# Kernel optimization log

Measured on AMD Instinct MI355X. Metric: run time of the kernel, lower is better.

Reference implementation:

```python
import jax, jax.numpy as jnp
import numpy as np

SIZE = 32
NUM_CLASSES = 10
B = 16384
RTOL = 0.01
ATOL = 0.01
MAX_STEPS = 96
H0 = 0.05


def setup_inputs() -> dict:
    key = jax.random.key(0)
    ks = jax.random.split(key, 9)
    p = lambda k, s: 0.1 * jax.random.normal(k, s, dtype=jnp.float32)
    z = lambda n: jnp.zeros((n,), dtype=jnp.float32)
    x = jax.random.normal(ks[0], (B, 2), dtype=jnp.float32)
    # per-sample ODE end times T_i in (0, 3]
    samples = 3.0 * jax.random.uniform(ks[1], (B, 1), dtype=jnp.float32) + 1e-3
    return dict(
        x=x, samples=samples,
        node_w1=p(ks[2], (3, SIZE)), node_b1=z(SIZE),
        node_w2=p(ks[3], (SIZE, SIZE)), node_b2=z(SIZE),
        node_w3=p(ks[4], (SIZE, 2)), node_b3=z(2),
        fc_w=p(ks[5], (2, NUM_CLASSES)), fc_b=z(NUM_CLASSES),
        enc_w1=p(ks[6], (2, SIZE)), enc_b1=z(SIZE),
        enc_w2=p(ks[7], (SIZE, SIZE)), enc_b2=z(SIZE),
        enc_w3=p(ks[8], (SIZE, 2)), enc_b3=z(2),
    )


def _net_forward(x, samples, node_w1, node_b1, node_w2, node_b2, node_w3, node_b3,
                 fc_w, fc_b, enc_w1, enc_b1, enc_w2, enc_b2, enc_w3, enc_b3):
    # Encoder -> (alpha, beta) feed only the external prob_model (no effect on act_vec)
    h = jax.nn.relu(x @ enc_w1 + enc_b1)
    h = jax.nn.relu(h @ enc_w2 + enc_b2)
    ab = h @ enc_w3 + enc_b3
    alpha, beta = jnp.exp(ab[:, 0]), jnp.exp(ab[:, 1])  # unused downstream (side effects only)

    # samples[samples >= 50] = 50
    T = jnp.minimum(samples[:, 0], 50.0)  # [B] per-sample end times

    def f(t, y):  # NODE dynamics; t: [B], y: [B,2]
        zin = jnp.concatenate([t[:, None], y], axis=1)  # [B,3]
        h1 = jax.nn.relu(zin @ node_w1 + node_b1)
        h2 = jax.nn.relu(h1 @ node_w2 + node_b2)
        return h2 @ node_w3 + node_b3  # [B,2]

    def step(carry, _):
        t, y, hstep = carry
        rem = T - t
        active = rem > 1e-8
        hs = jnp.where(active, jnp.minimum(hstep, rem), 0.0)  # never overshoot T
        hb = hs[:, None]
        # Dopri5 (RK45) stages
        k1 = f(t, y)
        k2 = f(t + hs * 0.2, y + hb * (0.2 * k1))
        k3 = f(t + hs * 0.3, y + hb * (3.0 / 40.0 * k1 + 9.0 / 40.0 * k2))
        k4 = f(t + hs * 0.8, y + hb * (44.0 / 45.0 * k1 - 56.0 / 15.0 * k2 + 32.0 / 9.0 * k3))
        k5 = f(t + hs * (8.0 / 9.0), y + hb * (19372.0 / 6561.0 * k1 - 25360.0 / 2187.0 * k2 + 64448.0 / 6561.0 * k3 - 212.0 / 729.0 * k4))
        k6 = f(t + hs, y + hb * (9017.0 / 3168.0 * k1 - 355.0 / 33.0 * k2 + 46732.0 / 5247.0 * k3 + 49.0 / 176.0 * k4 - 5103.0 / 18656.0 * k5))
        y5 = y + hb * (35.0 / 384.0 * k1 + 500.0 / 1113.0 * k3 + 125.0 / 192.0 * k4 - 2187.0 / 6784.0 * k5 + 11.0 / 84.0 * k6)
        k7 = f(t + hs, y5)
        err = hb * (71.0 / 57600.0 * k1 - 71.0 / 16695.0 * k3 + 71.0 / 1920.0 * k4 - 17253.0 / 339200.0 * k5 + 22.0 / 525.0 * k6 - 1.0 / 40.0 * k7)
        scale = ATOL + RTOL * jnp.maximum(jnp.abs(y), jnp.abs(y5))
        en = jnp.sqrt(jnp.mean((err / scale) ** 2, axis=1))  # [B]
        accept = active & (en <= 1.0)
        fac = jnp.clip(0.9 * jnp.maximum(en, 1e-10) ** (-0.2), 0.2, 10.0)
        t_n = jnp.where(accept, t + hs, t)
        y_n = jnp.where(accept[:, None], y5, y)
        h_n = jnp.where(active, hs * fac, hstep)
        return (t_n, y_n, h_n), None

    t0 = jnp.zeros((x.shape[0],), dtype=x.dtype)
    h0 = jnp.full((x.shape[0],), H0, dtype=x.dtype)
    (tF, yF, hF), _ = jax.lax.scan(step, (t0, x, h0), None, length=MAX_STEPS)

    # temp[idx] = flow of x[idx] from t=0 to its own T[idx] (sort/scatter in the
    # original only routes each sample's own interpolated state back to its row)
    act = yF @ fc_w + fc_b  # [B, num_classes]
    return act[None, :, :]  # act_vec: [1, B, num_classes]


def reference(x, samples, node_w1, node_b1, node_w2, node_b2, node_w3, node_b3,
              fc_w, fc_b, enc_w1, enc_b1, enc_w2, enc_b2, enc_w3, enc_b3):
    return _net_forward(x, samples, node_w1, node_b1, node_w2, node_b2, node_w3, node_b3,
                        fc_w, fc_b, enc_w1, enc_b1, enc_w2, enc_b2, enc_w3, enc_b3)
```

## Files before the change

kernel.cpp:

```cpp
#include <hip/hip_runtime.h>
#include <math.h>


#define MAXS 96

typedef float v2f __attribute__((ext_vector_type(2)));

static __device__ __forceinline__ v2f splat(float s) { v2f v; v.x = s; v.y = s; return v; }
static __device__ __forceinline__ v2f vfma(v2f a, v2f b, v2f c) { return __builtin_elementwise_fma(a, b, c); }
static __device__ __forceinline__ v2f vrelu(v2f a) { return __builtin_elementwise_max(a, splat(0.0f)); }

template<int CTRL>
static __device__ __forceinline__ float dppf(float x) {
    return __int_as_float(__builtin_amdgcn_update_dpp(
        0, __float_as_int(x), CTRL, 0xF, 0xF, false));
}

static __device__ __forceinline__ v2f dpp_allreduce16(v2f p) {
    p.x += dppf<0xB1>(p.x);  p.y += dppf<0xB1>(p.y);
    p.x += dppf<0x4E>(p.x);  p.y += dppf<0x4E>(p.y);
    p.x += dppf<0x141>(p.x); p.y += dppf<0x141>(p.y);
    p.x += dppf<0x140>(p.x); p.y += dppf<0x140>(p.y);
    return p;
}

__global__ __launch_bounds__(256, 3) void node_kernel(
    const float* __restrict__ x, const float* __restrict__ samples,
    const float* __restrict__ w1, const float* __restrict__ b1,
    const float* __restrict__ w2, const float* __restrict__ b2,
    const float* __restrict__ w3, const float* __restrict__ b3,
    const float* __restrict__ fcw, const float* __restrict__ fcb,
    float* __restrict__ out, int n)
{
    const int tid  = blockIdx.x * blockDim.x + threadIdx.x;
    const int elem = tid >> 4;
    const int m    = tid & 15;
    if (elem >= n) return;

    __shared__ float lds[16 * 36];
    float* slot = &lds[(threadIdx.x >> 4) * 36];

    const v2f* w1v = (const v2f*)w1;
    const v2f* b1v = (const v2f*)b1;
    const v2f* w2v = (const v2f*)w2;
    const v2f* b2v = (const v2f*)b2;
    const v2f* w3v = (const v2f*)w3;

    v2f w1r0 = w1v[0 * 16 + m];
    v2f w1r1 = w1v[1 * 16 + m];
    v2f w1r2 = w1v[2 * 16 + m];
    v2f b1c  = b1v[m];
    v2f b2c  = b2v[m];
    v2f w3r0 = w3v[2 * m + 0];
    v2f w3r1 = w3v[2 * m + 1];
    v2f b3c  = { b3[0], b3[1] };

    v2f w2c[32];
#pragma unroll
    for (int i = 0; i < 32; ++i) w2c[i] = w2v[i * 16 + m];

#pragma unroll
    for (int i = 0; i < 32; ++i) { asm volatile("" : "+v"(w2c[i])); }
    asm volatile("" : "+v"(w1r0), "+v"(w1r1), "+v"(w1r2), "+v"(b1c), "+v"(b2c));
    asm volatile("" : "+v"(w3r0), "+v"(w3r1));

    v2f y = ((const v2f*)x)[elem];
    float T = fminf(samples[elem], 50.0f);
    float t = 0.0f;
    float h = 0.05f;

    auto f_eval = [&](float tt, v2f z) -> v2f {
        v2f hv = vfma(splat(tt), w1r0, vfma(splat(z.x), w1r1,
                 vfma(splat(z.y), w1r2, b1c)));
        hv = vrelu(hv);

        ((v2f*)slot)[m] = hv;

        const float4* gp = (const float4*)slot;
        float4 r0 = gp[0], r1 = gp[1], r2 = gp[2], r3 = gp[3];
        float4 r4 = gp[4], r5 = gp[5], r6 = gp[6], r7 = gp[7];

        v2f a0 = b2c, a1 = splat(0.0f), a2 = splat(0.0f), a3 = splat(0.0f);
        a0 = vfma(splat(r0.x), w2c[ 0], a0); a1 = vfma(splat(r0.y), w2c[ 1], a1);
        a2 = vfma(splat(r0.z), w2c[ 2], a2); a3 = vfma(splat(r0.w), w2c[ 3], a3);
        a0 = vfma(splat(r1.x), w2c[ 4], a0); a1 = vfma(splat(r1.y), w2c[ 5], a1);
        a2 = vfma(splat(r1.z), w2c[ 6], a2); a3 = vfma(splat(r1.w), w2c[ 7], a3);
        a0 = vfma(splat(r2.x), w2c[ 8], a0); a1 = vfma(splat(r2.y), w2c[ 9], a1);
        a2 = vfma(splat(r2.z), w2c[10], a2); a3 = vfma(splat(r2.w), w2c[11], a3);
        a0 = vfma(splat(r3.x), w2c[12], a0); a1 = vfma(splat(r3.y), w2c[13], a1);
        a2 = vfma(splat(r3.z), w2c[14], a2); a3 = vfma(splat(r3.w), w2c[15], a3);
        a0 = vfma(splat(r4.x), w2c[16], a0); a1 = vfma(splat(r4.y), w2c[17], a1);
        a2 = vfma(splat(r4.z), w2c[18], a2); a3 = vfma(splat(r4.w), w2c[19], a3);
        a0 = vfma(splat(r5.x), w2c[20], a0); a1 = vfma(splat(r5.y), w2c[21], a1);
        a2 = vfma(splat(r5.z), w2c[22], a2); a3 = vfma(splat(r5.w), w2c[23], a3);
        a0 = vfma(splat(r6.x), w2c[24], a0); a1 = vfma(splat(r6.y), w2c[25], a1);
        a2 = vfma(splat(r6.z), w2c[26], a2); a3 = vfma(splat(r6.w), w2c[27], a3);
        a0 = vfma(splat(r7.x), w2c[28], a0); a1 = vfma(splat(r7.y), w2c[29], a1);
        a2 = vfma(splat(r7.z), w2c[30], a2); a3 = vfma(splat(r7.w), w2c[31], a3);

        v2f acc = vrelu((a0 + a1) + (a2 + a3));

        v2f p = vfma(splat(acc.x), w3r0, splat(acc.y) * w3r1);
        p = dpp_allreduce16(p);
        return p + b3c;
    };

    v2f k1 = f_eval(0.0f, y);

    for (int s = 0; s < MAXS; ++s) {
        float rem = T - t;
        if (!(rem > 1e-8f)) break;
        float hs = fminf(h, rem);
        v2f hb = splat(hs);

        v2f k2 = f_eval(t + hs * 0.2f, vfma(hb, splat(0.2f) * k1, y));
        v2f k3 = f_eval(t + hs * 0.3f,
                 vfma(hb, vfma(splat((float)(3.0/40.0)), k1, splat((float)(9.0/40.0)) * k2), y));
        v2f k4 = f_eval(t + hs * 0.8f,
                 vfma(hb, vfma(splat((float)(44.0/45.0)), k1,
                          vfma(splat((float)(-56.0/15.0)), k2, splat((float)(32.0/9.0)) * k3)), y));
        v2f k5 = f_eval(t + hs * (float)(8.0/9.0),
                 vfma(hb, vfma(splat((float)(19372.0/6561.0)), k1,
                          vfma(splat((float)(-25360.0/2187.0)), k2,
                          vfma(splat((float)(64448.0/6561.0)), k3,
                               splat((float)(-212.0/729.0)) * k4))), y));
        v2f k6 = f_eval(t + hs,
                 vfma(hb, vfma(splat((float)(9017.0/3168.0)), k1,
                          vfma(splat((float)(-355.0/33.0)), k2,
                          vfma(splat((float)(46732.0/5247.0)), k3,
                          vfma(splat((float)(49.0/176.0)), k4,
                               splat((float)(-5103.0/18656.0)) * k5)))), y));
        v2f y5 = vfma(hb, vfma(splat((float)(35.0/384.0)), k1,
                          vfma(splat((float)(500.0/1113.0)), k3,
                          vfma(splat((float)(125.0/192.0)), k4,
                          vfma(splat((float)(-2187.0/6784.0)), k5,
                               splat((float)(11.0/84.0)) * k6)))), y);
        v2f k7 = f_eval(t + hs, y5);

        v2f err = hb * vfma(splat((float)(71.0/57600.0)), k1,
                       vfma(splat((float)(-71.0/16695.0)), k3,
                       vfma(splat((float)(71.0/1920.0)), k4,
                       vfma(splat((float)(-17253.0/339200.0)), k5,
                       vfma(splat((float)(22.0/525.0)), k6,
                            splat((float)(-1.0/40.0)) * k7)))));

        v2f ay  = __builtin_elementwise_abs(y);
        v2f ay5 = __builtin_elementwise_abs(y5);
        v2f sc  = vfma(splat(0.01f), __builtin_elementwise_max(ay, ay5), splat(0.01f));
        v2f r   = err / sc;
        float en = sqrtf(0.5f * (r.x * r.x + r.y * r.y));

        float fac = 0.9f * powf(fmaxf(en, 1e-10f), -0.2f);
        fac = fminf(fmaxf(fac, 0.2f), 10.0f);

        bool accept = (en <= 1.0f);
        if (accept) { t += hs; y = y5; }
        k1 = accept ? k7 : k1;
        h = hs * fac;
    }

    if (m < 10) {
        out[10 * elem + m] = fmaf(y.x, fcw[m], fmaf(y.y, fcw[10 + m], fcb[m]));
    }
}

extern "C" void kernel_launch(void* const* d_in, const int* in_sizes, int n_in,
                              void* d_out, int out_size, void* d_ws, size_t ws_size,
                              hipStream_t stream) {
    const float* x   = (const float*)d_in[0];
    const float* sm  = (const float*)d_in[1];
    const float* w1  = (const float*)d_in[2];
    const float* b1  = (const float*)d_in[3];
    const float* w2  = (const float*)d_in[4];
    const float* b2  = (const float*)d_in[5];
    const float* w3  = (const float*)d_in[6];
    const float* b3  = (const float*)d_in[7];
    const float* fcw = (const float*)d_in[8];
    const float* fcb = (const float*)d_in[9];
    float* out = (float*)d_out;

    int n = in_sizes[1];
    const int block = 256;
    long long threads = (long long)n * 16;
    int grid = (int)((threads + block - 1) / block);
    node_kernel<<<grid, block, 0, stream>>>(x, sm, w1, b1, w2, b2, w3, b3,
                                            fcw, fcb, out, n);
}
```

Before: 105.6 us.

## Map each sample to 8 lanes with DPP quad broadcast plus LDS half-exchange

Each ODE sample is now handled by 8 lanes instead of 16, with each lane computing 4 hidden units and holding twice as many w2 weights in registers. Half of the hidden vector is gathered with DPP quad broadcasts and the other half is read from LDS, and the final reduction drops one DPP stage. This halves the total thread count and the per-sample duplicated step-control arithmetic, at the cost of much higher register use (occupancy hint lowered to 2) and a longer serial FMA chain per lane. The step-factor powf is replaced by exp2f/log2f.

Result: faster. 101.0 us, median of 2 (-4.4%).

```diff
diff --git a/kernel.cpp b/kernel.cpp
--- a/kernel.cpp
+++ b/kernel.cpp
@@ -6,25 +6,22 @@
 
 typedef float v2f __attribute__((ext_vector_type(2)));
 
-static __device__ __forceinline__ v2f splat(float s) { v2f v; v.x = s; v.y = s; return v; }
-static __device__ __forceinline__ v2f vfma(v2f a, v2f b, v2f c) { return __builtin_elementwise_fma(a, b, c); }
-static __device__ __forceinline__ v2f vrelu(v2f a) { return __builtin_elementwise_max(a, splat(0.0f)); }
+static __device__ __forceinline__ v2f splat(float s){ v2f v; v.x=s; v.y=s; return v; }
+static __device__ __forceinline__ v2f vfma(v2f a, v2f b, v2f c){ return __builtin_elementwise_fma(a,b,c); }
+static __device__ __forceinline__ v2f vrelu(v2f a){ return __builtin_elementwise_max(a, splat(0.0f)); }
 
 template<int CTRL>
-static __device__ __forceinline__ float dppf(float x) {
-    return __int_as_float(__builtin_amdgcn_update_dpp(
-        0, __float_as_int(x), CTRL, 0xF, 0xF, false));
-}
-
-static __device__ __forceinline__ v2f dpp_allreduce16(v2f p) {
+static __device__ __forceinline__ float dppf(float x){
+    return __int_as_float(__builtin_amdgcn_update_dpp(0, __float_as_int(x), CTRL, 0xF, 0xF, false));
+}
+static __device__ __forceinline__ v2f dpp_allreduce8(v2f p){
     p.x += dppf<0xB1>(p.x);  p.y += dppf<0xB1>(p.y);
     p.x += dppf<0x4E>(p.x);  p.y += dppf<0x4E>(p.y);
     p.x += dppf<0x141>(p.x); p.y += dppf<0x141>(p.y);
-    p.x += dppf<0x140>(p.x); p.y += dppf<0x140>(p.y);
     return p;
 }
 
-__global__ __launch_bounds__(256, 3) void node_kernel(
+__global__ __launch_bounds__(256, 2) void node_kernel(
     const float* __restrict__ x, const float* __restrict__ samples,
     const float* __restrict__ w1, const float* __restrict__ b1,
     const float* __restrict__ w2, const float* __restrict__ b2,
@@ -33,36 +30,48 @@
     float* __restrict__ out, int n)
 {
     const int tid  = blockIdx.x * blockDim.x + threadIdx.x;
-    const int elem = tid >> 4;
-    const int m    = tid & 15;
+    const int elem = tid >> 3;
+    const int m    = tid & 7;
     if (elem >= n) return;
-
-    __shared__ float lds[16 * 36];
-    float* slot = &lds[(threadIdx.x >> 4) * 36];
-
-    const v2f* w1v = (const v2f*)w1;
-    const v2f* b1v = (const v2f*)b1;
-    const v2f* w2v = (const v2f*)w2;
-    const v2f* b2v = (const v2f*)b2;
+    const int q = m >> 2;
+
+    __shared__ float lds[32 * 36];
+    float* slot = &lds[(threadIdx.x >> 3) * 36];
+    const int mineBase  = 16 * q;
+    const int otherBase = 16 - mineBase;
+
+    const float4* w2v4 = (const float4*)w2;
+    v2f w2mA[16], w2mB[16];
+    v2f w2oA[16], w2oB[16];
+#pragma unroll
+    for (int k = 0; k < 16; ++k) {
+        float4 rm = w2v4[(mineBase  + k) * 8 + m];
+        float4 ro = w2v4[(otherBase + k) * 8 + m];
+        w2mA[k].x = rm.x; w2mA[k].y = rm.y; w2mB[k].x = rm.z; w2mB[k].y = rm.w;
+        w2oA[k].x = ro.x; w2oA[k].y = ro.y; w2oB[k].x = ro.z; w2oB[k].y = ro.w;
+    }
+    float4 w1f0 = ((const float4*)w1)[0 * 8 + m];
+    float4 w1f1 = ((const float4*)w1)[1 * 8 + m];
+    float4 w1f2 = ((const float4*)w1)[2 * 8 + m];
+    float4 b1f  = ((const float4*)b1)[m];
+    float4 b2f  = ((const float4*)b2)[m];
+    v2f w1_0A = {w1f0.x, w1f0.y}, w1_0B = {w1f0.z, w1f0.w};
+    v2f w1_1A = {w1f1.x, w1f1.y}, w1_1B = {w1f1.z, w1f1.w};
+    v2f w1_2A = {w1f2.x, w1f2.y}, w1_2B = {w1f2.z, w1f2.w};
+    v2f b1A   = {b1f.x,  b1f.y }, b1B   = {b1f.z,  b1f.w };
+    v2f b2A   = {b2f.x,  b2f.y }, b2B   = {b2f.z,  b2f.w };
     const v2f* w3v = (const v2f*)w3;
-
-    v2f w1r0 = w1v[0 * 16 + m];
-    v2f w1r1 = w1v[1 * 16 + m];
-    v2f w1r2 = w1v[2 * 16 + m];
-    v2f b1c  = b1v[m];
-    v2f b2c  = b2v[m];
-    v2f w3r0 = w3v[2 * m + 0];
-    v2f w3r1 = w3v[2 * m + 1];
+    v2f w3r0 = w3v[4*m+0], w3r1 = w3v[4*m+1], w3r2 = w3v[4*m+2], w3r3 = w3v[4*m+3];
     v2f b3c  = { b3[0], b3[1] };
 
-    v2f w2c[32];
 #pragma unroll
-    for (int i = 0; i < 32; ++i) w2c[i] = w2v[i * 16 + m];
-
-#pragma unroll
-    for (int i = 0; i < 32; ++i) { asm volatile("" : "+v"(w2c[i])); }
-    asm volatile("" : "+v"(w1r0), "+v"(w1r1), "+v"(w1r2), "+v"(b1c), "+v"(b2c));
-    asm volatile("" : "+v"(w3r0), "+v"(w3r1));
+    for (int k = 0; k < 16; ++k) {
+        asm volatile("" : "+v"(w2mA[k]), "+v"(w2mB[k]), "+v"(w2oA[k]), "+v"(w2oB[k]));
+    }
+    asm volatile("" : "+v"(w1_0A), "+v"(w1_0B), "+v"(w1_1A), "+v"(w1_1B));
+    asm volatile("" : "+v"(w1_2A), "+v"(w1_2B), "+v"(b1A), "+v"(b1B));
+    asm volatile("" : "+v"(b2A), "+v"(b2B));
+    asm volatile("" : "+v"(w3r0), "+v"(w3r1), "+v"(w3r2), "+v"(w3r3));
 
     v2f y = ((const v2f*)x)[elem];
     float T = fminf(samples[elem], 50.0f);
@@ -70,38 +79,65 @@
     float h = 0.05f;
 
     auto f_eval = [&](float tt, v2f z) -> v2f {
-        v2f hv = vfma(splat(tt), w1r0, vfma(splat(z.x), w1r1,
-                 vfma(splat(z.y), w1r2, b1c)));
-        hv = vrelu(hv);
-
-        ((v2f*)slot)[m] = hv;
-
-        const float4* gp = (const float4*)slot;
-        float4 r0 = gp[0], r1 = gp[1], r2 = gp[2], r3 = gp[3];
-        float4 r4 = gp[4], r5 = gp[5], r6 = gp[6], r7 = gp[7];
-
-        v2f a0 = b2c, a1 = splat(0.0f), a2 = splat(0.0f), a3 = splat(0.0f);
-        a0 = vfma(splat(r0.x), w2c[ 0], a0); a1 = vfma(splat(r0.y), w2c[ 1], a1);
-        a2 = vfma(splat(r0.z), w2c[ 2], a2); a3 = vfma(splat(r0.w), w2c[ 3], a3);
-        a0 = vfma(splat(r1.x), w2c[ 4], a0); a1 = vfma(splat(r1.y), w2c[ 5], a1);
-        a2 = vfma(splat(r1.z), w2c[ 6], a2); a3 = vfma(splat(r1.w), w2c[ 7], a3);
-        a0 = vfma(splat(r2.x), w2c[ 8], a0); a1 = vfma(splat(r2.y), w2c[ 9], a1);
-        a2 = vfma(splat(r2.z), w2c[10], a2); a3 = vfma(splat(r2.w), w2c[11], a3);
-        a0 = vfma(splat(r3.x), w2c[12], a0); a1 = vfma(splat(r3.y), w2c[13], a1);
-        a2 = vfma(splat(r3.z), w2c[14], a2); a3 = vfma(splat(r3.w), w2c[15], a3);
-        a0 = vfma(splat(r4.x), w2c[16], a0); a1 = vfma(splat(r4.y), w2c[17], a1);
-        a2 = vfma(splat(r4.z), w2c[18], a2); a3 = vfma(splat(r4.w), w2c[19], a3);
-        a0 = vfma(splat(r5.x), w2c[20], a0); a1 = vfma(splat(r5.y), w2c[21], a1);
-        a2 = vfma(splat(r5.z), w2c[22], a2); a3 = vfma(splat(r5.w), w2c[23], a3);
-        a0 = vfma(splat(r6.x), w2c[24], a0); a1 = vfma(splat(r6.y), w2c[25], a1);
-        a2 = vfma(splat(r6.z), w2c[26], a2); a3 = vfma(splat(r6.w), w2c[27], a3);
-        a0 = vfma(splat(r7.x), w2c[28], a0); a1 = vfma(splat(r7.y), w2c[29], a1);
-        a2 = vfma(splat(r7.z), w2c[30], a2); a3 = vfma(splat(r7.w), w2c[31], a3);
-
-        v2f acc = vrelu((a0 + a1) + (a2 + a3));
-
-        v2f p = vfma(splat(acc.x), w3r0, splat(acc.y) * w3r1);
-        p = dpp_allreduce16(p);
+        v2f hA = vrelu(vfma(splat(tt), w1_0A, vfma(splat(z.x), w1_1A, vfma(splat(z.y), w1_2A, b1A))));
+        v2f hB = vrelu(vfma(splat(tt), w1_0B, vfma(splat(z.x), w1_1B, vfma(splat(z.y), w1_2B, b1B))));
+
+        float4 wv; wv.x = hA.x; wv.y = hA.y; wv.z = hB.x; wv.w = hB.y;
+        ((float4*)slot)[m] = wv;
+
+        float mg0  = dppf<0x00>(hA.x), mg1  = dppf<0x00>(hA.y),
+              mg2  = dppf<0x00>(hB.x), mg3  = dppf<0x00>(hB.y);
+        float mg4  = dppf<0x55>(hA.x), mg5  = dppf<0x55>(hA.y),
+              mg6  = dppf<0x55>(hB.x), mg7  = dppf<0x55>(hB.y);
+        float mg8  = dppf<0xAA>(hA.x), mg9  = dppf<0xAA>(hA.y),
+              mg10 = dppf<0xAA>(hB.x), mg11 = dppf<0xAA>(hB.y);
+        float mg12 = dppf<0xFF>(hA.x), mg13 = dppf<0xFF>(hA.y),
+              mg14 = dppf<0xFF>(hB.x), mg15 = dppf<0xFF>(hB.y);
+
+        const float4* op = (const float4*)(slot + otherBase);
+        float4 o0 = op[0], o1 = op[1], o2 = op[2], o3 = op[3];
+
+        v2f aA = b2A, aB = b2B, cA = splat(0.0f), cB = splat(0.0f);
+        aA = vfma(splat(mg0 ), w2mA[ 0], aA); aB = vfma(splat(mg0 ), w2mB[ 0], aB);
+        aA = vfma(splat(mg1 ), w2mA[ 1], aA); aB = vfma(splat(mg1 ), w2mB[ 1], aB);
+        aA = vfma(splat(mg2 ), w2mA[ 2], aA); aB = vfma(splat(mg2 ), w2mB[ 2], aB);
+        aA = vfma(splat(mg3 ), w2mA[ 3], aA); aB = vfma(splat(mg3 ), w2mB[ 3], aB);
+        aA = vfma(splat(mg4 ), w2mA[ 4], aA); aB = vfma(splat(mg4 ), w2mB[ 4], aB);
+        aA = vfma(splat(mg5 ), w2mA[ 5], aA); aB = vfma(splat(mg5 ), w2mB[ 5], aB);
+        aA = vfma(splat(mg6 ), w2mA[ 6], aA); aB = vfma(splat(mg6 ), w2mB[ 6], aB);
+        aA = vfma(splat(mg7 ), w2mA[ 7], aA); aB = vfma(splat(mg7 ), w2mB[ 7], aB);
+        aA = vfma(splat(mg8 ), w2mA[ 8], aA); aB = vfma(splat(mg8 ), w2mB[ 8], aB);
+        aA = vfma(splat(mg9 ), w2mA[ 9], aA); aB = vfma(splat(mg9 ), w2mB[ 9], aB);
+        aA = vfma(splat(mg10), w2mA[10], aA); aB = vfma(splat(mg10), w2mB[10], aB);
+        aA = vfma(splat(mg11), w2mA[11], aA); aB = vfma(splat(mg11), w2mB[11], aB);
+        aA = vfma(splat(mg12), w2mA[12], aA); aB = vfma(splat(mg12), w2mB[12], aB);
+        aA = vfma(splat(mg13), w2mA[13], aA); aB = vfma(splat(mg13), w2mB[13], aB);
+        aA = vfma(splat(mg14), w2mA[14], aA); aB = vfma(splat(mg14), w2mB[14], aB);
+        aA = vfma(splat(mg15), w2mA[15], aA); aB = vfma(splat(mg15), w2mB[15], aB);
+        cA = vfma(splat(o0.x), w2oA[ 0], cA); cB = vfma(splat(o0.x), w2oB[ 0], cB);
+        cA = vfma(splat(o0.y), w2oA[ 1], cA); cB = vfma(splat(o0.y), w2oB[ 1], cB);
+        cA = vfma(splat(o0.z), w2oA[ 2], cA); cB = vfma(splat(o0.z), w2oB[ 2], cB);
+        cA = vfma(splat(o0.w), w2oA[ 3], cA); cB = vfma(splat(o0.w), w2oB[ 3], cB);
+        cA = vfma(splat(o1.x), w2oA[ 4], cA); cB = vfma(splat(o1.x), w2oB[ 4], cB);
+        cA = vfma(splat(o1.y), w2oA[ 5], cA); cB = vfma(splat(o1.y), w2oB[ 5], cB);
+        cA = vfma(splat(o1.z), w2oA[ 6], cA); cB = vfma(splat(o1.z), w2oB[ 6], cB);
+        cA = vfma(splat(o1.w), w2oA[ 7], cA); cB = vfma(splat(o1.w), w2oB[ 7], cB);
+        cA = vfma(splat(o2.x), w2oA[ 8], cA); cB = vfma(splat(o2.x), w2oB[ 8], cB);
+        cA = vfma(splat(o2.y), w2oA[ 9], cA); cB = vfma(splat(o2.y), w2oB[ 9], cB);
+        cA = vfma(splat(o2.z), w2oA[10], cA); cB = vfma(splat(o2.z), w2oB[10], cB);
+        cA = vfma(splat(o2.w), w2oA[11], cA); cB = vfma(splat(o2.w), w2oB[11], cB);
+        cA = vfma(splat(o3.x), w2oA[12], cA); cB = vfma(splat(o3.x), w2oB[12], cB);
+        cA = vfma(splat(o3.y), w2oA[13], cA); cB = vfma(splat(o3.y), w2oB[13], cB);
+        cA = vfma(splat(o3.z), w2oA[14], cA); cB = vfma(splat(o3.z), w2oB[14], cB);
+        cA = vfma(splat(o3.w), w2oA[15], cA); cB = vfma(splat(o3.w), w2oB[15], cB);
+
+        v2f h2A = vrelu(aA + cA);
+        v2f h2B = vrelu(aB + cB);
+
+        v2f p = vfma(splat(h2A.x), w3r0,
+                vfma(splat(h2A.y), w3r1,
+                vfma(splat(h2B.x), w3r2, splat(h2B.y) * w3r3)));
+        p = dpp_allreduce8(p);
         return p + b3c;
     };
 
@@ -144,14 +180,13 @@
                        vfma(splat((float)(22.0/525.0)), k6,
                             splat((float)(-1.0/40.0)) * k7)))));
 
-        v2f ay  = __builtin_elementwise_abs(y);
-        v2f ay5 = __builtin_elementwise_abs(y5);
-        v2f sc  = vfma(splat(0.01f), __builtin_elementwise_max(ay, ay5), splat(0.01f));
-        v2f r   = err / sc;
+        v2f sc = vfma(splat(0.01f),
+                 __builtin_elementwise_max(__builtin_elementwise_abs(y),
+                                           __builtin_elementwise_abs(y5)), splat(0.01f));
+        v2f r = err / sc;
         float en = sqrtf(0.5f * (r.x * r.x + r.y * r.y));
 
-        float fac = 0.9f * powf(fmaxf(en, 1e-10f), -0.2f);
-        fac = fminf(fmaxf(fac, 0.2f), 10.0f);
+        float fac = fminf(fmaxf(0.9f * exp2f(-0.2f * log2f(fmaxf(en, 1e-10f))), 0.2f), 10.0f);
 
         bool accept = (en <= 1.0f);
         if (accept) { t += hs; y = y5; }
@@ -159,8 +194,10 @@
         h = hs * fac;
     }
 
-    if (m < 10) {
-        out[10 * elem + m] = fmaf(y.x, fcw[m], fmaf(y.y, fcw[10 + m], fcb[m]));
+    out[10 * elem + m] = fmaf(y.x, fcw[m], fmaf(y.y, fcw[10 + m], fcb[m]));
+    if (m < 2) {
+        int c = 8 + m;
+        out[10 * elem + c] = fmaf(y.x, fcw[c], fmaf(y.y, fcw[10 + c], fcb[c]));
     }
 }
 
@@ -181,7 +218,7 @@
 
     int n = in_sizes[1];
     const int block = 256;
-    long long threads = (long long)n * 16;
+    long long threads = (long long)n * 8;
     int grid = (int)((threads + block - 1) / block);
     node_kernel<<<grid, block, 0, stream>>>(x, sm, w1, b1, w2, b2, w3, b3,
                                             fcw, fcb, out, n);
```

## Spread each sample over 32 lanes with one hidden unit per lane

Applied to the files above, without the earlier changes.

Each ODE sample now uses 32 threads instead of 16, and each thread owns one hidden unit rather than a pair. Per-thread register use for W2 drops from 64 to 32 floats, which permits raising launch bounds to 4 blocks per SM. The output reduction gains a ds_swizzle stage so it spans 32 lanes. The grid doubles and redundant scalar step-control work is duplicated across more lanes. powf is replaced by exp2/log2.

Result: slower. 112.1 us (+6.2%).

```diff
diff --git a/kernel.cpp b/kernel.cpp
--- a/kernel.cpp
+++ b/kernel.cpp
@@ -6,25 +6,27 @@
 
 typedef float v2f __attribute__((ext_vector_type(2)));
 
-static __device__ __forceinline__ v2f splat(float s) { v2f v; v.x = s; v.y = s; return v; }
-static __device__ __forceinline__ v2f vfma(v2f a, v2f b, v2f c) { return __builtin_elementwise_fma(a, b, c); }
-static __device__ __forceinline__ v2f vrelu(v2f a) { return __builtin_elementwise_max(a, splat(0.0f)); }
+static __device__ __forceinline__ v2f splat(float s){ v2f v; v.x=s; v.y=s; return v; }
+static __device__ __forceinline__ v2f vfma(v2f a, v2f b, v2f c){ return __builtin_elementwise_fma(a,b,c); }
+static __device__ __forceinline__ v2f vrelu(v2f a){ return __builtin_elementwise_max(a, splat(0.0f)); }
 
 template<int CTRL>
-static __device__ __forceinline__ float dppf(float x) {
-    return __int_as_float(__builtin_amdgcn_update_dpp(
-        0, __float_as_int(x), CTRL, 0xF, 0xF, false));
+static __device__ __forceinline__ float dppf(float x){
+    return __int_as_float(__builtin_amdgcn_update_dpp(0, __float_as_int(x), CTRL, 0xF, 0xF, false));
 }
-
-static __device__ __forceinline__ v2f dpp_allreduce16(v2f p) {
+static __device__ __forceinline__ float swz16(float x){
+    return __int_as_float(__builtin_amdgcn_ds_swizzle(__float_as_int(x), 0x401F));
+}
+static __device__ __forceinline__ v2f allreduce32(v2f p){
     p.x += dppf<0xB1>(p.x);  p.y += dppf<0xB1>(p.y);
     p.x += dppf<0x4E>(p.x);  p.y += dppf<0x4E>(p.y);
     p.x += dppf<0x141>(p.x); p.y += dppf<0x141>(p.y);
     p.x += dppf<0x140>(p.x); p.y += dppf<0x140>(p.y);
+    p.x += swz16(p.x);       p.y += swz16(p.y);
     return p;
 }
 
-__global__ __launch_bounds__(256, 3) void node_kernel(
+__global__ __launch_bounds__(256, 4) void node_kernel(
     const float* __restrict__ x, const float* __restrict__ samples,
     const float* __restrict__ w1, const float* __restrict__ b1,
     const float* __restrict__ w2, const float* __restrict__ b2,
@@ -33,36 +35,25 @@
     float* __restrict__ out, int n)
 {
     const int tid  = blockIdx.x * blockDim.x + threadIdx.x;
-    const int elem = tid >> 4;
-    const int m    = tid & 15;
+    const int elem = tid >> 5;
+    const int m    = tid & 31;
     if (elem >= n) return;
 
-    __shared__ float lds[16 * 36];
-    float* slot = &lds[(threadIdx.x >> 4) * 36];
+    __shared__ float lds[8 * 36];
+    float* slot = &lds[(threadIdx.x >> 5) * 36];
 
-    const v2f* w1v = (const v2f*)w1;
-    const v2f* b1v = (const v2f*)b1;
-    const v2f* w2v = (const v2f*)w2;
-    const v2f* b2v = (const v2f*)b2;
-    const v2f* w3v = (const v2f*)w3;
-
-    v2f w1r0 = w1v[0 * 16 + m];
-    v2f w1r1 = w1v[1 * 16 + m];
-    v2f w1r2 = w1v[2 * 16 + m];
-    v2f b1c  = b1v[m];
-    v2f b2c  = b2v[m];
-    v2f w3r0 = w3v[2 * m + 0];
-    v2f w3r1 = w3v[2 * m + 1];
-    v2f b3c  = { b3[0], b3[1] };
-
-    v2f w2c[32];
+    float w2c[32];
 #pragma unroll
-    for (int i = 0; i < 32; ++i) w2c[i] = w2v[i * 16 + m];
+    for (int j = 0; j < 32; ++j) w2c[j] = w2[j * 32 + m];
+    float w1c0 = w1[ 0 + m], w1c1 = w1[32 + m], w1c2 = w1[64 + m];
+    float b1c  = b1[m], b2c = b2[m];
+    v2f   w3c; w3c.x = w3[2*m + 0]; w3c.y = w3[2*m + 1];
+    v2f   b3c; b3c.x = b3[0]; b3c.y = b3[1];
 
 #pragma unroll
-    for (int i = 0; i < 32; ++i) { asm volatile("" : "+v"(w2c[i])); }
-    asm volatile("" : "+v"(w1r0), "+v"(w1r1), "+v"(w1r2), "+v"(b1c), "+v"(b2c));
-    asm volatile("" : "+v"(w3r0), "+v"(w3r1));
+    for (int j = 0; j < 32; ++j) { asm volatile("" : "+v"(w2c[j])); }
+    asm volatile("" : "+v"(w1c0), "+v"(w1c1), "+v"(w1c2), "+v"(b1c), "+v"(b2c));
+    asm volatile("" : "+v"(w3c));
 
     v2f y = ((const v2f*)x)[elem];
     float T = fminf(samples[elem], 50.0f);
@@ -70,38 +61,29 @@
     float h = 0.05f;
 
     auto f_eval = [&](float tt, v2f z) -> v2f {
-        v2f hv = vfma(splat(tt), w1r0, vfma(splat(z.x), w1r1,
-                 vfma(splat(z.y), w1r2, b1c)));
-        hv = vrelu(hv);
+        float hv = fmaxf(fmaf(tt, w1c0, fmaf(z.x, w1c1, fmaf(z.y, w1c2, b1c))), 0.0f);
 
-        ((v2f*)slot)[m] = hv;
+        slot[m] = hv;
 
         const float4* gp = (const float4*)slot;
-        float4 r0 = gp[0], r1 = gp[1], r2 = gp[2], r3 = gp[3];
-        float4 r4 = gp[4], r5 = gp[5], r6 = gp[6], r7 = gp[7];
 
-        v2f a0 = b2c, a1 = splat(0.0f), a2 = splat(0.0f), a3 = splat(0.0f);
-        a0 = vfma(splat(r0.x), w2c[ 0], a0); a1 = vfma(splat(r0.y), w2c[ 1], a1);
-        a2 = vfma(splat(r0.z), w2c[ 2], a2); a3 = vfma(splat(r0.w), w2c[ 3], a3);
-        a0 = vfma(splat(r1.x), w2c[ 4], a0); a1 = vfma(splat(r1.y), w2c[ 5], a1);
-        a2 = vfma(splat(r1.z), w2c[ 6], a2); a3 = vfma(splat(r1.w), w2c[ 7], a3);
-        a0 = vfma(splat(r2.x), w2c[ 8], a0); a1 = vfma(splat(r2.y), w2c[ 9], a1);
-        a2 = vfma(splat(r2.z), w2c[10], a2); a3 = vfma(splat(r2.w), w2c[11], a3);
-        a0 = vfma(splat(r3.x), w2c[12], a0); a1 = vfma(splat(r3.y), w2c[13], a1);
-        a2 = vfma(splat(r3.z), w2c[14], a2); a3 = vfma(splat(r3.w), w2c[15], a3);
-        a0 = vfma(splat(r4.x), w2c[16], a0); a1 = vfma(splat(r4.y), w2c[17], a1);
-        a2 = vfma(splat(r4.z), w2c[18], a2); a3 = vfma(splat(r4.w), w2c[19], a3);
-        a0 = vfma(splat(r5.x), w2c[20], a0); a1 = vfma(splat(r5.y), w2c[21], a1);
-        a2 = vfma(splat(r5.z), w2c[22], a2); a3 = vfma(splat(r5.w), w2c[23], a3);
-        a0 = vfma(splat(r6.x), w2c[24], a0); a1 = vfma(splat(r6.y), w2c[25], a1);
-        a2 = vfma(splat(r6.z), w2c[26], a2); a3 = vfma(splat(r6.w), w2c[27], a3);
-        a0 = vfma(splat(r7.x), w2c[28], a0); a1 = vfma(splat(r7.y), w2c[29], a1);
-        a2 = vfma(splat(r7.z), w2c[30], a2); a3 = vfma(splat(r7.w), w2c[31], a3);
+        float a0 = b2c, a1 = 0.0f, a2 = 0.0f, a3 = 0.0f;
+#pragma unroll
+        for (int j = 0; j < 8; j += 4) {
+            float4 r0 = gp[j], r1 = gp[j+1], r2 = gp[j+2], r3 = gp[j+3];
+            a0 = fmaf(r0.x, w2c[4*j +  0], a0); a1 = fmaf(r0.y, w2c[4*j +  1], a1);
+            a2 = fmaf(r0.z, w2c[4*j +  2], a2); a3 = fmaf(r0.w, w2c[4*j +  3], a3);
+            a0 = fmaf(r1.x, w2c[4*j +  4], a0); a1 = fmaf(r1.y, w2c[4*j +  5], a1);
+            a2 = fmaf(r1.z, w2c[4*j +  6], a2); a3 = fmaf(r1.w, w2c[4*j +  7], a3);
+            a0 = fmaf(r2.x, w2c[4*j +  8], a0); a1 = fmaf(r2.y, w2c[4*j +  9], a1);
+            a2 = fmaf(r2.z, w2c[4*j + 10], a2); a3 = fmaf(r2.w, w2c[4*j + 11], a3);
+            a0 = fmaf(r3.x, w2c[4*j + 12], a0); a1 = fmaf(r3.y, w2c[4*j + 13], a1);
+            a2 = fmaf(r3.z, w2c[4*j + 14], a2); a3 = fmaf(r3.w, w2c[4*j + 15], a3);
+        }
+        float h2 = fmaxf((a0 + a1) + (a2 + a3), 0.0f);
 
-        v2f acc = vrelu((a0 + a1) + (a2 + a3));
-
-        v2f p = vfma(splat(acc.x), w3r0, splat(acc.y) * w3r1);
-        p = dpp_allreduce16(p);
+        v2f p = splat(h2) * w3c;
+        p = allreduce32(p);
         return p + b3c;
     };
 
@@ -144,14 +126,13 @@
                        vfma(splat((float)(22.0/525.0)), k6,
                             splat((float)(-1.0/40.0)) * k7)))));
 
-        v2f ay  = __builtin_elementwise_abs(y);
-        v2f ay5 = __builtin_elementwise_abs(y5);
-        v2f sc  = vfma(splat(0.01f), __builtin_elementwise_max(ay, ay5), splat(0.01f));
-        v2f r   = err / sc;
+        v2f sc = vfma(splat(0.01f),
+                 __builtin_elementwise_max(__builtin_elementwise_abs(y),
+                                           __builtin_elementwise_abs(y5)), splat(0.01f));
+        v2f r = err / sc;
         float en = sqrtf(0.5f * (r.x * r.x + r.y * r.y));
 
-        float fac = 0.9f * powf(fmaxf(en, 1e-10f), -0.2f);
-        fac = fminf(fmaxf(fac, 0.2f), 10.0f);
+        float fac = fminf(fmaxf(0.9f * exp2f(-0.2f * log2f(fmaxf(en, 1e-10f))), 0.2f), 10.0f);
 
         bool accept = (en <= 1.0f);
         if (accept) { t += hs; y = y5; }
@@ -181,7 +162,7 @@
 
     int n = in_sizes[1];
     const int block = 256;
-    long long threads = (long long)n * 16;
+    long long threads = (long long)n * 32;
     int grid = (int)((threads + block - 1) / block);
     node_kernel<<<grid, block, 0, stream>>>(x, sm, w1, b1, w2, b2, w3, b3,
                                             fcw, fcb, out, n);
```
